# Kernel optimization log

Hardware: AMD Instinct MI355X
Metric: run time of the kernel (lower is better)

Reference implementation:

```python
import jax, jax.numpy as jnp
import numpy as np

# ---- module hyperparameters (match init_kwargs) ----
B = 4            # number of point clouds (equal-sized for jit-friendliness)
NB = 4096        # points per cloud; N = B*NB = 16384
N = B * NB
D_IN = 64        # feature dim of x
RATIO = 0.25
MB = int(RATIO * NB)   # 1024 sampled centroids per cloud
R = 0.2                # ball radius
K = 64                 # max_num_neighbors
MLP = [D_IN + 3, 128, 128, 256]


def setup_inputs() -> dict:
    key = jax.random.key(0)
    ks = jax.random.split(key, 8)
    x = jax.random.normal(ks[0], (N, D_IN), dtype=jnp.float32)
    pos = jax.random.uniform(ks[1], (N, 3), dtype=jnp.float32)  # unit cube
    batch = (jnp.arange(N, dtype=jnp.int32) // NB)              # equal-sized clouds
    def lin(k, fan_in, fan_out):
        w = jax.random.normal(k, (fan_in, fan_out), dtype=jnp.float32) * (1.0 / np.sqrt(fan_in))
        b = jnp.zeros((fan_out,), dtype=jnp.float32)
        return w, b
    W1, b1 = lin(ks[2], MLP[0], MLP[1])
    W2, b2 = lin(ks[3], MLP[1], MLP[2])
    W3, b3 = lin(ks[4], MLP[2], MLP[3])
    return {"x": x, "pos": pos, "batch": batch,
            "W1": W1, "b1": b1, "W2": W2, "b2": b2, "W3": W3, "b3": b3}


def _fps_one(p):
    """Farthest point sampling on one cloud p:[NB,3] -> [MB] indices (start at 0)."""
    def body(k, state):
        sel, dist = state
        last = p[sel[k - 1]]                               # [3]
        d2 = jnp.sum((p - last) ** 2, axis=-1)             # [NB]
        dist = jnp.minimum(dist, d2)
        sel = sel.at[k].set(jnp.argmax(dist).astype(jnp.int32))
        return sel, dist
    sel0 = jnp.zeros((MB,), dtype=jnp.int32)
    dist0 = jnp.full((NB,), jnp.inf, dtype=p.dtype)
    sel, _ = jax.lax.fori_loop(1, MB, body, (sel0, dist0))
    return sel


def _radius_one(p, sel):
    """For each centroid, first K in-ball neighbor indices (by index order, like torch_cluster.radius)."""
    q = p[sel]                                              # [MB,3]
    d2 = jnp.sum((q[:, None, :] - p[None, :, :]) ** 2, -1) # [MB,NB]
    mask = d2 <= R * R
    order_key = jnp.where(mask, jnp.arange(NB, dtype=jnp.int32)[None, :], NB)
    nbr = jnp.argsort(order_key, axis=1)[:, :K]            # [MB,K] first-K in-ball
    valid = jnp.take_along_axis(mask, nbr, axis=1)          # [MB,K]
    return nbr, valid


def _conv_one(p, xb, sel, nbr, valid, W1, b1, W2, b2, W3, b3):
    """PointNetConv: msg = MLP(cat(x_j, pos_j - pos_i)), max-aggregated over the ball."""
    q = p[sel]                                   # [MB,3]
    rel = p[nbr] - q[:, None, :]                 # [MB,K,3]
    feat = jnp.concatenate([xb[nbr], rel], -1)   # [MB,K,67]
    h = jax.nn.relu(jnp.einsum('mki,io->mko', feat, W1) + b1)
    h = jax.nn.relu(jnp.einsum('mki,io->mko', h, W2) + b2)
    h = jax.nn.relu(jnp.einsum('mki,io->mko', h, W3) + b3)
    h = jnp.where(valid[..., None], h, -1e9)
    return jnp.max(h, axis=1)                    # [MB,256]


def reference(x, pos, batch, W1, b1, W2, b2, W3, b3):
    # batch is arange(N)//NB: clouds are contiguous and equal-sized -> reshape.
    pos_b = pos.reshape(B, NB, 3)
    x_b = x.reshape(B, NB, D_IN)
    sel = jax.vmap(_fps_one)(pos_b)                         # [B,MB]
    nbr, valid = jax.vmap(_radius_one)(pos_b, sel)          # [B,MB,K]
    out = jax.vmap(_conv_one, in_axes=(0, 0, 0, 0, 0, None, None, None, None, None, None))(
        pos_b, x_b, sel, nbr, valid, W1, b1, W2, b2, W3, b3)  # [B,MB,256]
    x_out = out.reshape(B * MB, MLP[-1])
    pos_out = jnp.take_along_axis(pos_b, sel[..., None], axis=1).reshape(B * MB, 3)
    batch_out = jnp.repeat(jnp.arange(B, dtype=jnp.int32), MB)
    return x_out, pos_out, batch_out
```

## Files before the change

kernel.cpp:

```cpp
#include <hip/hip_runtime.h>

typedef unsigned int UI;
typedef unsigned long long ULL;
typedef _Float16 f16;
typedef _Float16 h8 __attribute__((ext_vector_type(8)));
typedef float f32x4 __attribute__((ext_vector_type(4)));
typedef float fl2 __attribute__((ext_vector_type(2)));

#define NB_PTS 4096
#define MB_SEL 1024
#define KNBR   64
#define NCLOUD 4
#define NCENT  4096

#define WT2_OFF 12288
#define WT3_OFF 28672
#define WS_ELEMS 61440
#define WSFLAG_MAGIC 0x1234ABCDu

#define OFF_H1   13312
#define OFF_H2   30720
#define OFF_PMAX 48128
#define OFF_MASK 49152
#define OFF_NBR  49664
#define OFF_NV   49920
#define OFF_SHS  49924
#define OFF_SLOT 65536
#define DYN_LDS  86016

__device__ __forceinline__ double d2_np64(double dx, double dy, double dz) {
  return __dadd_rn(__dadd_rn(__dmul_rn(dx, dx), __dmul_rn(dy, dy)),
                   __dmul_rn(dz, dz));
}

template <int CTRL>
__device__ __forceinline__ ULL dpp_max_step(ULL cur) {
  UI lo = (UI)cur, hi = (UI)(cur >> 32);
  UI nl = (UI)__builtin_amdgcn_update_dpp(0, (int)lo, CTRL, 0xf, 0xf, true);
  UI nh = (UI)__builtin_amdgcn_update_dpp(0, (int)hi, CTRL, 0xf, 0xf, true);
  ULL nv = ((ULL)nh << 32) | (ULL)nl;
  return nv > cur ? nv : cur;
}

__global__ __launch_bounds__(512, 2) void fused_kernel(
    const float* __restrict__ x, const float* __restrict__ pos,
    const float* __restrict__ W1, const float* __restrict__ b1,
    const float* __restrict__ W2, const float* __restrict__ b2,
    const float* __restrict__ W3, const float* __restrict__ b3,
    f16* __restrict__ ws, UI* __restrict__ wsflag,
    float* __restrict__ selstash, float* __restrict__ out_x,
    float* __restrict__ out_pos, float* __restrict__ out_batch) {
  extern __shared__ char smem[];
  const int tid  = threadIdx.x;
  const int lane = tid & 63;
  const int wv   = tid >> 6;

  if (blockIdx.x == NCLOUD) {
    for (int t = tid; t < WS_ELEMS; t += 512) {
      if (t < WT2_OFF) {
        int n = t / 96, k = t - n * 96;
        ws[t] = (k < 67) ? (f16)W1[k * 128 + n] : (f16)0.f;
      } else if (t < WT3_OFF) {
        int u = t - WT2_OFF;
        int n = u >> 7, k = u & 127;
        ws[t] = (f16)W2[k * 128 + n];
      } else {
        int u = t - WT3_OFF;
        int n = u >> 7, k = u & 127;
        ws[t] = (f16)W3[k * 256 + n];
      }
    }
    __syncthreads();
    if (tid == 0)
      __hip_atomic_store(wsflag, WSFLAG_MAGIC, __ATOMIC_RELEASE,
                         __HIP_MEMORY_SCOPE_AGENT);
    return;
  }

  if (blockIdx.x < NCLOUD) {
#pragma clang fp contract(off)
    asm volatile("s_setprio 3");
    float4* pp = (float4*)smem;
    ULL* slots = (ULL*)(smem + OFF_SLOT);
    const int b = blockIdx.x;

    fl2 mx[4], my[4], mz[4], dist[4];
#pragma unroll
    for (int t = 0; t < 4; ++t) {
      int j0 = tid + (2 * t) * 512;
      int j1 = tid + (2 * t + 1) * 512;
      size_t a0 = ((size_t)b * NB_PTS + j0) * 3;
      size_t a1 = ((size_t)b * NB_PTS + j1) * 3;
      float X0 = pos[a0], Y0 = pos[a0 + 1], Z0 = pos[a0 + 2];
      float X1 = pos[a1], Y1 = pos[a1 + 1], Z1 = pos[a1 + 2];
      pp[j0] = make_float4(X0, Y0, Z0, 0.f);
      pp[j1] = make_float4(X1, Y1, Z1, 0.f);
      mx[t] = fl2{X0, X1}; my[t] = fl2{Y0, Y1}; mz[t] = fl2{Z0, Z1};
      dist[t] = fl2{__builtin_inff(), __builtin_inff()};
    }
    if (tid == 0)
      __hip_atomic_store(&selstash[b * MB_SEL], 1.0f, __ATOMIC_RELAXED,
                         __HIP_MEMORY_SCOPE_AGENT);
    __syncthreads();

    int cur = 0;
    for (int k = 1; k < MB_SEL; ++k) {
      float4 w = pp[cur];
      float bestv = -__builtin_inff();
      int   besti = 0x7fffffff;
#pragma unroll
      for (int t = 0; t < 4; ++t) {
        fl2 dx = mx[t] - w.x;
        fl2 dy = my[t] - w.y;
        fl2 dz = mz[t] - w.z;
        fl2 dd = (dx * dx + dy * dy) + dz * dz;
        fl2 dc = dist[t];
        float d0 = fminf(dc.x, dd.x);
        float d1 = fminf(dc.y, dd.y);
        dist[t] = fl2{d0, d1};
        if (d0 > bestv) { bestv = d0; besti = tid + (2 * t) * 512; }
        if (d1 > bestv) { bestv = d1; besti = tid + (2 * t + 1) * 512; }
      }
      ULL key = ((ULL)__float_as_uint(bestv) << 32) | (ULL)(~(UI)besti);
      key = dpp_max_step<0x111>(key);
      key = dpp_max_step<0x112>(key);
      key = dpp_max_step<0x114>(key);
      key = dpp_max_step<0x118>(key);
      key = dpp_max_step<0x142>(key);
      key = dpp_max_step<0x143>(key);
      const int buf = (k & 1) * 8;
      if (lane == 63) slots[buf + wv] = key;
      __syncthreads();
      const ULL* sp = slots + buf;
      ULL s0 = sp[0], s1 = sp[1], s2 = sp[2], s3 = sp[3];
      ULL s4 = sp[4], s5 = sp[5], s6 = sp[6], s7 = sp[7];
      ULL m01 = s0 > s1 ? s0 : s1;
      ULL m23 = s2 > s3 ? s2 : s3;
      ULL m45 = s4 > s5 ? s4 : s5;
      ULL m67 = s6 > s7 ? s6 : s7;
      ULL ma = m01 > m23 ? m01 : m23;
      ULL mb = m45 > m67 ? m45 : m67;
      ULL mk = ma > mb ? ma : mb;
      int winner = (int)(~(UI)mk);
      if (tid == 0)
        __hip_atomic_store(&selstash[b * MB_SEL + k], (float)(winner + 1),
                           __ATOMIC_RELAXED, __HIP_MEMORY_SCOPE_AGENT);
      cur = winner;
    }
    return;
  }

  f16* featA  = (f16*)smem;
  f16* h1s    = (f16*)(smem + OFF_H1);
  f16* h2s    = (f16*)(smem + OFF_H2);
  float* pmax = (float*)(smem + OFF_PMAX);
  ULL* masks  = (ULL*)(smem + OFF_MASK);
  int* nbrS   = (int*)(smem + OFF_NBR);
  int* nvP    = (int*)(smem + OFF_NV);
  int* shS    = (int*)(smem + OFF_SHS);

  const int c  = (int)blockIdx.x - (NCLOUD + 1);
  const int k  = c >> 2;
  const int b  = c & 3;
  const int cg = b * MB_SEL + k;

  if (tid == 0) {
    while (__hip_atomic_load(wsflag, __ATOMIC_ACQUIRE,
                             __HIP_MEMORY_SCOPE_AGENT) != WSFLAG_MAGIC)
      __builtin_amdgcn_s_sleep(2);
  }
  __syncthreads();

  const int n    = lane & 15;
  const int quad = lane >> 4;
  const int col  = wv * 16 + n;
  h8 B1f[3], B2f[4];
  float bv1, bv2, bv3[2];
  bv1 = b1[col];
  bv2 = b2[col];
#pragma unroll
  for (int kt = 0; kt < 3; ++kt)
    B1f[kt] = *(const h8*)(ws + col * 96 + kt * 32 + quad * 8);
#pragma unroll
  for (int kt = 0; kt < 4; ++kt)
    B2f[kt] = *(const h8*)(ws + WT2_OFF + col * 128 + kt * 32 + quad * 8);
#pragma unroll
  for (int ct = 0; ct < 2; ++ct) bv3[ct] = b3[(2 * wv + ct) * 16 + n];

  if (tid == 0) {
    float v;
    for (;;) {
      v = __hip_atomic_load(&selstash[cg], __ATOMIC_RELAXED,
                            __HIP_MEMORY_SCOPE_AGENT);
      if (v >= 1.0f) break;
      __builtin_amdgcn_s_sleep(8);
    }
    *shS = (int)v - 1;
  }
  __syncthreads();
  const int s = (*shS) & (NB_PTS - 1);

  const size_t qb = ((size_t)(b * NB_PTS + s)) * 3;
  const float qxf = pos[qb], qyf = pos[qb + 1], qzf = pos[qb + 2];
  const double qx = (double)qxf, qy = (double)qyf, qz = (double)qzf;
  const double RR = 0.2 * 0.2;

#pragma unroll
  for (int it = 0; it < 8; ++it) {
    const int ch = wv * 8 + it;
    const int j  = ch * 64 + lane;
    const size_t pb = ((size_t)b * NB_PTS + j) * 3;
    double d2 = d2_np64((double)pos[pb] - qx, (double)pos[pb + 1] - qy,
                        (double)pos[pb + 2] - qz);
    ULL m = __ballot(d2 <= RR);
    if (lane == 0) masks[ch] = m;
  }
  __syncthreads();

  if (tid < 64) {
    ULL m = masks[tid];
    int pc = __popcll(m);
    int incl = pc;
#pragma unroll
    for (int off = 1; off < 64; off <<= 1) {
      int o = __shfl_up(incl, off, 64);
      if (tid >= off) incl += o;
    }
    int base = incl - pc;
    int tot  = __shfl(incl, 63, 64);
    int nvw  = min(tot, KNBR);
    if (tid == 63) *nvP = nvw;
    int slot = base;
    ULL mm = m;
    while (mm && slot < KNBR) {
      int bit = __ffsll(mm) - 1;
      nbrS[slot++] = tid * 64 + bit;
      mm &= mm - 1;
    }
    if (tid >= nvw) nbrS[tid] = s;
  }
  __syncthreads();
  const int nv = *nvP;

  {
    const int r = tid >> 3;
    const int part = tid & 7;
    const int g = nbrS[r];
    const float* xrow = x + (((size_t)(b * NB_PTS + g)) << 6) + part * 8;
    float4 u0 = *(const float4*)(xrow);
    float4 u1 = *(const float4*)(xrow + 4);
    h8 o0;
    o0[0]=(f16)u0.x; o0[1]=(f16)u0.y; o0[2]=(f16)u0.z; o0[3]=(f16)u0.w;
    o0[4]=(f16)u1.x; o0[5]=(f16)u1.y; o0[6]=(f16)u1.z; o0[7]=(f16)u1.w;
    *(h8*)(featA + r * 104 + part * 8) = o0;
    if (part == 7) {
      size_t gb = ((size_t)(b * NB_PTS + g)) * 3;
      h8 rv = {(f16)0.f,(f16)0.f,(f16)0.f,(f16)0.f,(f16)0.f,(f16)0.f,(f16)0.f,(f16)0.f};
      rv[0] = (f16)(pos[gb]     - qxf);
      rv[1] = (f16)(pos[gb + 1] - qyf);
      rv[2] = (f16)(pos[gb + 2] - qzf);
      h8 z = {(f16)0.f,(f16)0.f,(f16)0.f,(f16)0.f,(f16)0.f,(f16)0.f,(f16)0.f,(f16)0.f};
      *(h8*)(featA + r * 104 + 64) = rv;
      *(h8*)(featA + r * 104 + 72) = z;
      *(h8*)(featA + r * 104 + 80) = z;
      *(h8*)(featA + r * 104 + 88) = z;
    }
  }
  __syncthreads();

#pragma unroll
  for (int at = 0; at < 4; ++at) {
    f32x4 acc = {0.f, 0.f, 0.f, 0.f};
#pragma unroll
    for (int kt = 0; kt < 3; ++kt) {
      h8 a = *(const h8*)(featA + (at * 16 + n) * 104 + kt * 32 + quad * 8);
      acc = __builtin_amdgcn_mfma_f32_16x16x32_f16(a, B1f[kt], acc, 0, 0, 0);
    }
#pragma unroll
    for (int r = 0; r < 4; ++r)
      h1s[(at * 16 + quad * 4 + r) * 136 + col] = (f16)fmaxf(acc[r] + bv1, 0.f);
  }
  __syncthreads();

#pragma unroll
  for (int at = 0; at < 4; ++at) {
    f32x4 acc = {0.f, 0.f, 0.f, 0.f};
#pragma unroll
    for (int kt = 0; kt < 4; ++kt) {
      h8 a = *(const h8*)(h1s + (at * 16 + n) * 136 + kt * 32 + quad * 8);
      acc = __builtin_amdgcn_mfma_f32_16x16x32_f16(a, B2f[kt], acc, 0, 0, 0);
    }
#pragma unroll
    for (int r = 0; r < 4; ++r)
      h2s[(at * 16 + quad * 4 + r) * 136 + col] = (f16)fmaxf(acc[r] + bv2, 0.f);
  }
  __syncthreads();

  float vm[2] = {0.f, 0.f};
#pragma unroll
  for (int at = 0; at < 4; ++at) {
#pragma unroll
    for (int ct = 0; ct < 2; ++ct) {
      const int c3 = (2 * wv + ct) * 16 + n;
      f32x4 acc = {0.f, 0.f, 0.f, 0.f};
#pragma unroll
      for (int kt = 0; kt < 4; ++kt) {
        h8 a = *(const h8*)(h2s + (at * 16 + n) * 136 + kt * 32 + quad * 8);
        h8 wfr = *(const h8*)(ws + WT3_OFF + c3 * 128 + kt * 32 + quad * 8);
        acc = __builtin_amdgcn_mfma_f32_16x16x32_f16(a, wfr, acc, 0, 0, 0);
      }
#pragma unroll
      for (int r = 0; r < 4; ++r) {
        float h = fmaxf(acc[r] + bv3[ct], 0.f);
        const int row = at * 16 + quad * 4 + r;
        vm[ct] = fmaxf(vm[ct], row < nv ? h : 0.f);
      }
    }
  }
#pragma unroll
  for (int ct = 0; ct < 2; ++ct) {
    vm[ct] = fmaxf(vm[ct], __shfl_xor(vm[ct], 16, 64));
    vm[ct] = fmaxf(vm[ct], __shfl_xor(vm[ct], 32, 64));
  }
  if (quad == 0) {
#pragma unroll
    for (int ct = 0; ct < 2; ++ct) pmax[(2 * wv + ct) * 16 + n] = vm[ct];
  }
  __syncthreads();

  if (tid < 256) out_x[(size_t)cg * 256 + tid] = pmax[tid];
  if (tid < 3) out_pos[cg * 3 + tid] = pos[qb + tid];
  if (tid == 0) out_batch[cg] = (float)b;
}

extern "C" void kernel_launch(void* const* d_in, const int* in_sizes, int n_in,
                              void* d_out, int out_size, void* d_ws, size_t ws_size,
                              hipStream_t stream) {
  const float* x   = (const float*)d_in[0];
  const float* pos = (const float*)d_in[1];
  const float* W1 = (const float*)d_in[3];
  const float* b1 = (const float*)d_in[4];
  const float* W2 = (const float*)d_in[5];
  const float* b2 = (const float*)d_in[6];
  const float* W3 = (const float*)d_in[7];
  const float* b3 = (const float*)d_in[8];

  float* out = (float*)d_out;
  float* out_pos   = out + (size_t)NCENT * 256;
  float* out_batch = out_pos + (size_t)NCENT * 3;
  f16* ws    = (f16*)d_ws;
  UI* wsflag = (UI*)((char*)d_ws + 2 * WS_ELEMS);

  hipFuncSetAttribute((const void*)fused_kernel,
                      hipFuncAttributeMaxDynamicSharedMemorySize, DYN_LDS);

  fused_kernel<<<NCLOUD + 1 + NCENT, 512, DYN_LDS, stream>>>(
      x, pos, W1, b1, W2, b2, W3, b3, ws, wsflag,
      out_batch, out, out_pos, out_batch);
}
```

Before: 724.6 us.

## Run FPS on four waves with more points per thread and lighter barrier

```diff
diff --git a/kernel.cpp b/kernel.cpp
--- a/kernel.cpp
+++ b/kernel.cpp
@@ -80,15 +80,21 @@
   if (blockIdx.x < NCLOUD) {
 #pragma clang fp contract(off)
     asm volatile("s_setprio 3");
+    const int b = blockIdx.x;
+
+    if (wv >= 4) {
+      for (int k = 1; k < MB_SEL; ++k) __builtin_amdgcn_s_barrier();
+      return;
+    }
+
     float4* pp = (float4*)smem;
     ULL* slots = (ULL*)(smem + OFF_SLOT);
-    const int b = blockIdx.x;
-
-    fl2 mx[4], my[4], mz[4], dist[4];
-#pragma unroll
-    for (int t = 0; t < 4; ++t) {
-      int j0 = tid + (2 * t) * 512;
-      int j1 = tid + (2 * t + 1) * 512;
+
+    fl2 mx[8], my[8], mz[8], dist[8];
+#pragma unroll
+    for (int t = 0; t < 8; ++t) {
+      int j0 = tid + (2 * t) * 256;
+      int j1 = tid + (2 * t + 1) * 256;
       size_t a0 = ((size_t)b * NB_PTS + j0) * 3;
       size_t a1 = ((size_t)b * NB_PTS + j1) * 3;
       float X0 = pos[a0], Y0 = pos[a0 + 1], Z0 = pos[a0 + 2];
@@ -101,51 +107,47 @@
     if (tid == 0)
       __hip_atomic_store(&selstash[b * MB_SEL], 1.0f, __ATOMIC_RELAXED,
                          __HIP_MEMORY_SCOPE_AGENT);
-    __syncthreads();
-
-    int cur = 0;
+
+    const size_t qb0 = (size_t)b * NB_PTS * 3;
+    float wx = pos[qb0], wy = pos[qb0 + 1], wz = pos[qb0 + 2];
+
     for (int k = 1; k < MB_SEL; ++k) {
-      float4 w = pp[cur];
       float bestv = -__builtin_inff();
-      int   besti = 0x7fffffff;
-#pragma unroll
-      for (int t = 0; t < 4; ++t) {
-        fl2 dx = mx[t] - w.x;
-        fl2 dy = my[t] - w.y;
-        fl2 dz = mz[t] - w.z;
+      UI    bestn = 0;
+#pragma unroll
+      for (int t = 0; t < 8; ++t) {
+        fl2 dx = mx[t] - wx;
+        fl2 dy = my[t] - wy;
+        fl2 dz = mz[t] - wz;
         fl2 dd = (dx * dx + dy * dy) + dz * dz;
         fl2 dc = dist[t];
         float d0 = fminf(dc.x, dd.x);
         float d1 = fminf(dc.y, dd.y);
         dist[t] = fl2{d0, d1};
-        if (d0 > bestv) { bestv = d0; besti = tid + (2 * t) * 512; }
-        if (d1 > bestv) { bestv = d1; besti = tid + (2 * t + 1) * 512; }
+        if (d0 > bestv) { bestv = d0; bestn = ~(UI)(tid + (2 * t) * 256); }
+        if (d1 > bestv) { bestv = d1; bestn = ~(UI)(tid + (2 * t + 1) * 256); }
       }
-      ULL key = ((ULL)__float_as_uint(bestv) << 32) | (ULL)(~(UI)besti);
+      ULL key = ((ULL)__float_as_uint(bestv) << 32) | (ULL)bestn;
       key = dpp_max_step<0x111>(key);
       key = dpp_max_step<0x112>(key);
       key = dpp_max_step<0x114>(key);
       key = dpp_max_step<0x118>(key);
       key = dpp_max_step<0x142>(key);
       key = dpp_max_step<0x143>(key);
-      const int buf = (k & 1) * 8;
+      const int buf = (k & 1) * 4;
       if (lane == 63) slots[buf + wv] = key;
-      __syncthreads();
+      asm volatile("s_waitcnt lgkmcnt(0)\n\ts_barrier" ::: "memory");
       const ULL* sp = slots + buf;
       ULL s0 = sp[0], s1 = sp[1], s2 = sp[2], s3 = sp[3];
-      ULL s4 = sp[4], s5 = sp[5], s6 = sp[6], s7 = sp[7];
       ULL m01 = s0 > s1 ? s0 : s1;
       ULL m23 = s2 > s3 ? s2 : s3;
-      ULL m45 = s4 > s5 ? s4 : s5;
-      ULL m67 = s6 > s7 ? s6 : s7;
-      ULL ma = m01 > m23 ? m01 : m23;
-      ULL mb = m45 > m67 ? m45 : m67;
-      ULL mk = ma > mb ? ma : mb;
+      ULL mk  = m01 > m23 ? m01 : m23;
       int winner = (int)(~(UI)mk);
       if (tid == 0)
         __hip_atomic_store(&selstash[b * MB_SEL + k], (float)(winner + 1),
                            __ATOMIC_RELAXED, __HIP_MEMORY_SCOPE_AGENT);
-      cur = winner;
+      float4 w4 = pp[winner];
+      wx = w4.x; wy = w4.y; wz = w4.z;
     }
     return;
   }
```

New measurement: 1.123 ms. 55.0% more time.
